# Optimization experiments

Measured on AMD Instinct MI355X. Metric: run time of the kernel, lower is better.

## Reference

```python
import jax, jax.numpy as jnp
import numpy as np

B, S, D, H = 8, 1024, 768, 12
DK = D // H  # 64


def setup_inputs() -> dict:
    key = jax.random.key(0)
    ks = jax.random.split(key, 11)
    scale = 1.0 / np.sqrt(D)
    inp = {
        "query": jax.random.normal(ks[0], (B, S, D), jnp.float32),
        "key": jax.random.normal(ks[1], (B, S, D), jnp.float32),
        "value": jax.random.normal(ks[2], (B, S, D), jnp.float32),
        "Wq": jax.random.normal(ks[3], (D, D), jnp.float32) * scale,
        "bq": jnp.zeros((D,), jnp.float32),
        "Wk": jax.random.normal(ks[4], (D, D), jnp.float32) * scale,
        "bk": jnp.zeros((D,), jnp.float32),
        "Wv": jax.random.normal(ks[5], (D, D), jnp.float32) * scale,
        "bv": jnp.zeros((D,), jnp.float32),
        "Wd": jax.random.normal(ks[6], (D, D), jnp.float32) * scale,
        "bd": jnp.zeros((D,), jnp.float32),
    }
    return inp


def reference(query, key, value, Wq, bq, Wk, bk, Wv, bv, Wd, bd):
    # QKV projections (torch Linear equivalent: x @ W + b with W stored [in,out])
    q = query @ Wq + bq  # [B,S,D]
    k = key @ Wk + bk
    v = value @ Wv + bv
    # split heads -> [B,H,S,DK]
    q = q.reshape(B, S, H, DK).transpose(0, 2, 1, 3)
    k = k.reshape(B, S, H, DK).transpose(0, 2, 1, 3)
    v = v.reshape(B, S, H, DK).transpose(0, 2, 1, 3)
    scores = jnp.einsum("bhqd,bhkd->bhqk", q, k) / jnp.sqrt(jnp.float32(DK))
    weights = jax.nn.softmax(scores, axis=-1)  # attn dropout = identity (eval)
    ctx = jnp.einsum("bhqk,bhkd->bhqd", weights, v)
    context = ctx.transpose(0, 2, 1, 3).reshape(B, S, D)
    hidden_states = context @ Wd + bd  # out dropout = identity (eval)
    return (hidden_states, context)
```

## Files before the change

kernel.cpp:

```cpp
#include <hip/hip_runtime.h>
#include <hip/hip_bf16.h>
#include <math.h>

constexpr int Bc = 8;
constexpr int Sc = 1024;
constexpr int Dc = 768;
constexpr int Hc = 12;
constexpr int DKc = 64;
constexpr int BSc = Bc * Sc;
constexpr size_t HEAD_ELEMS = (size_t)Bc * Hc * Sc * DKc;
constexpr size_t OUT_ELEMS  = (size_t)Bc * Sc * Dc;

typedef __attribute__((ext_vector_type(8))) short short8;
typedef __attribute__((ext_vector_type(4))) short short4v;
typedef __attribute__((ext_vector_type(4))) float f32x4;

__device__ __forceinline__ short f2bf(float x) {
  __hip_bfloat16 h = __float2bfloat16(x);
  short r;
  __builtin_memcpy(&r, &h, 2);
  return r;
}

__device__ __forceinline__ void gload16(const void* g, void* l) {
  __builtin_amdgcn_global_load_lds(
      (const __attribute__((address_space(1))) void*)g,
      (__attribute__((address_space(3))) void*)l, 16, 0, 0);
}

__global__ __launch_bounds__(256) void wtrans(
    const float* __restrict__ W, __hip_bfloat16* __restrict__ Wt) {
  __shared__ float t[32][33];
  const int tx = threadIdx.x & 31, ty = threadIdx.x >> 5;
  const int bx = blockIdx.x * 32;
  const int by = blockIdx.y * 32;
  #pragma unroll
  for (int i = 0; i < 32; i += 8)
    t[ty + i][tx] = W[(size_t)(by + ty + i) * Dc + bx + tx];
  __syncthreads();
  #pragma unroll
  for (int i = 0; i < 32; i += 8)
    Wt[(size_t)(bx + ty + i) * Dc + by + tx] = __float2bfloat16(t[tx][ty + i]);
}

template <int MODE>
__global__ __launch_bounds__(256) void gemm_mfma(
    const float* __restrict__ A, const __hip_bfloat16* __restrict__ Wt,
    const float* __restrict__ bias, void* __restrict__ out) {
  __shared__ __hip_bfloat16 As[128 * 64];
  __shared__ __hip_bfloat16 Bs[128 * 64];

  const int tid = threadIdx.x;
  const int lane = tid & 63;
  const int wv = tid >> 6;
  const int l15 = lane & 15;
  const int g = lane >> 4;
  const int wr = wv >> 1, wc = wv & 1;

  const int nwg = gridDim.x;
  const int orig = blockIdx.x;
  const int swz = (orig & 7) * (nwg >> 3) + (orig >> 3);
  const int rb = swz / (Dc / 128);
  const int cb = swz % (Dc / 128);
  const int row0 = rb * 128, col0 = cb * 128;

  f32x4 acc[4][4];
  #pragma unroll
  for (int ai = 0; ai < 4; ai++)
    #pragma unroll
    for (int bj = 0; bj < 4; bj++) acc[ai][bj] = f32x4{0.f, 0.f, 0.f, 0.f};

  for (int k0 = 0; k0 < Dc; k0 += 64) {
    __syncthreads();

    #pragma unroll
    for (int j = 0; j < 4; j++) {
      const int r = j * 32 + wv * 8 + (lane >> 3);
      const __hip_bfloat16* gp =
          Wt + (size_t)(col0 + r) * Dc + k0 + (lane & 7) * 8;
      gload16(gp, &Bs[(j * 32 + wv * 8) * 64]);
    }

    #pragma unroll
    for (int i = 0; i < 4; i++) {
      const int id = tid + i * 256;
      const int r = id >> 3, gi = id & 7;
      const float* ap = A + (size_t)(row0 + r) * Dc + k0 + gi * 8;
      const float4 f0 = *reinterpret_cast<const float4*>(ap);
      const float4 f1 = *reinterpret_cast<const float4*>(ap + 4);
      short8 s;
      s[0] = f2bf(f0.x); s[1] = f2bf(f0.y); s[2] = f2bf(f0.z); s[3] = f2bf(f0.w);
      s[4] = f2bf(f1.x); s[5] = f2bf(f1.y); s[6] = f2bf(f1.z); s[7] = f2bf(f1.w);
      *reinterpret_cast<short8*>(&As[r * 64 + gi * 8]) = s;
    }
    __syncthreads();

    #pragma unroll
    for (int kk = 0; kk < 2; kk++) {
      short8 a[4], b[4];
      #pragma unroll
      for (int ai = 0; ai < 4; ai++)
        a[ai] = *reinterpret_cast<const short8*>(
            &As[(wr * 64 + ai * 16 + l15) * 64 + kk * 32 + g * 8]);
      #pragma unroll
      for (int bj = 0; bj < 4; bj++)
        b[bj] = *reinterpret_cast<const short8*>(
            &Bs[(wc * 64 + bj * 16 + l15) * 64 + kk * 32 + g * 8]);
      #pragma unroll
      for (int ai = 0; ai < 4; ai++)
        #pragma unroll
        for (int bj = 0; bj < 4; bj++) {
          if constexpr (MODE == 2)
            acc[ai][bj] = __builtin_amdgcn_mfma_f32_16x16x32_bf16(
                b[bj], a[ai], acc[ai][bj], 0, 0, 0);
          else
            acc[ai][bj] = __builtin_amdgcn_mfma_f32_16x16x32_bf16(
                a[ai], b[bj], acc[ai][bj], 0, 0, 0);
        }
    }
  }

  const int mb = row0 + wr * 64, nb = col0 + wc * 64;
  #pragma unroll
  for (int ai = 0; ai < 4; ai++)
    #pragma unroll
    for (int bj = 0; bj < 4; bj++)
      #pragma unroll
      for (int reg = 0; reg < 4; reg++) {
        const float v = acc[ai][bj][reg];
        if constexpr (MODE == 2) {
          const int n = nb + bj * 16 + g * 4 + reg;
          const int m = mb + ai * 16 + l15;
          const float val = v + bias[n];
          const int b_ = m >> 10, s_ = m & 1023;
          const int h_ = n >> 6, dk = n & 63;
          ((__hip_bfloat16*)out)[(((size_t)(b_ * Hc + h_)) * DKc + dk) * Sc + s_] =
              __float2bfloat16(val);
        } else {
          const int m = mb + ai * 16 + g * 4 + reg;
          const int n = nb + bj * 16 + l15;
          const float val = v + bias[n];
          if constexpr (MODE == 0) {
            const int b_ = m >> 10, s_ = m & 1023;
            const int h_ = n >> 6, dk = n & 63;
            ((__hip_bfloat16*)out)[(((size_t)(b_ * Hc + h_)) * Sc + s_) * DKc + dk] =
                __float2bfloat16(val);
          } else {
            ((float*)out)[(size_t)m * Dc + n] = val;
          }
        }
      }
}

__global__ __launch_bounds__(256) void attn_mfma(
    const __hip_bfloat16* __restrict__ Q, const __hip_bfloat16* __restrict__ K,
    const __hip_bfloat16* __restrict__ Vt, float* __restrict__ ctx) {
  __shared__ __hip_bfloat16 Ks[64 * 64];
  __shared__ __hip_bfloat16 Vs[64 * 64];

  const int tid = threadIdx.x;
  const int lane = tid & 63;
  const int w = tid >> 6;
  const int l15 = lane & 15;
  const int g = lane >> 4;

  const int cpx = gridDim.x >> 3;
  const int bid = blockIdx.x;
  const int wid = (bid & 7) * cpx + (bid >> 3);
  const int bh = wid >> 4;
  const int qt = wid & 15;
  const int qbase = qt * 64 + w * 16;

  const __hip_bfloat16* Qb = Q + (size_t)bh * Sc * DKc;
  const __hip_bfloat16* Kb = K + (size_t)bh * Sc * DKc;
  const __hip_bfloat16* Vtb = Vt + (size_t)bh * DKc * Sc;

  short8 qf[2];
  {
    const __hip_bfloat16* qp = Qb + (size_t)(qbase + l15) * DKc + g * 8;
    qf[0] = *reinterpret_cast<const short8*>(qp);
    qf[1] = *reinterpret_cast<const short8*>(qp + 32);
  }

  f32x4 Oacc[4];
  #pragma unroll
  for (int dt = 0; dt < 4; dt++) Oacc[dt] = f32x4{0.f, 0.f, 0.f, 0.f};
  float m_run = -1e30f, l_run = 0.f;

  constexpr float SM_SCALE = 0.125f * 1.44269504088896340736f;

  for (int kt = 0; kt < Sc; kt += 64) {
    __syncthreads();
    #pragma unroll
    for (int it = 0; it < 2; it++) {
      const int tt = tid + it * 256;
      const int row = tt >> 3, s = tt & 7;
      const float4 kv = *reinterpret_cast<const float4*>(
          Kb + (size_t)(kt + row) * DKc + s * 8);
      const float4 vv = *reinterpret_cast<const float4*>(
          Vtb + (size_t)row * Sc + kt + s * 8);
      const int off = row * 128 + ((s ^ (row & 7)) << 4);
      *reinterpret_cast<float4*>((char*)Ks + off) = kv;
      *reinterpret_cast<float4*>((char*)Vs + off) = vv;
    }
    __syncthreads();

    f32x4 sacc[4];
    #pragma unroll
    for (int mt = 0; mt < 4; mt++) sacc[mt] = f32x4{0.f, 0.f, 0.f, 0.f};
    #pragma unroll
    for (int c = 0; c < 2; c++) {
      #pragma unroll
      for (int mt = 0; mt < 4; mt++) {
        const int row = mt * 16 + l15;
        const short8 kf = *reinterpret_cast<const short8*>(
            (char*)Ks + row * 128 + (((g + 4 * c) ^ (row & 7)) << 4));
        sacc[mt] =
            __builtin_amdgcn_mfma_f32_16x16x32_bf16(kf, qf[c], sacc[mt], 0, 0, 0);
      }
    }

    float tmax = -1e30f;
    #pragma unroll
    for (int s = 0; s < 4; s++)
      #pragma unroll
      for (int r = 0; r < 4; r++) tmax = fmaxf(tmax, sacc[s][r]);
    tmax = fmaxf(tmax, __shfl_xor(tmax, 16));
    tmax = fmaxf(tmax, __shfl_xor(tmax, 32));
    const float mnew = fmaxf(m_run, tmax);
    const float alpha = __builtin_amdgcn_exp2f((m_run - mnew) * SM_SCALE);
    m_run = mnew;
    float wgt[4][4];
    float wsum = 0.f;
    #pragma unroll
    for (int s = 0; s < 4; s++)
      #pragma unroll
      for (int r = 0; r < 4; r++) {
        wgt[s][r] = __builtin_amdgcn_exp2f((sacc[s][r] - mnew) * SM_SCALE);
        wsum += wgt[s][r];
      }
    l_run = l_run * alpha + wsum;

    float ar[4];
    #pragma unroll
    for (int r = 0; r < 4; r++) ar[r] = __shfl(alpha, g * 4 + r);
    #pragma unroll
    for (int dt = 0; dt < 4; dt++)
      #pragma unroll
      for (int r = 0; r < 4; r++) Oacc[dt][r] *= ar[r];

    short8 pa[2];
    #pragma unroll
    for (int c = 0; c < 2; c++)
      #pragma unroll
      for (int i = 0; i < 8; i++) pa[c][i] = f2bf(wgt[2 * c + (i >> 2)][i & 3]);

    #pragma unroll
    for (int dt = 0; dt < 4; dt++) {
      const int row = dt * 16 + l15;
      const int rb2 = row * 128;
      const int sw = row & 7;
      const int gl = (g & 1) * 8;
      const int gh = g >> 1;
      #pragma unroll
      for (int c = 0; c < 2; c++) {
        const short4v v0 = *reinterpret_cast<const short4v*>(
            (char*)Vs + rb2 + ((((4 * c + 0) + gh) ^ sw) << 4) + gl);
        const short4v v1 = *reinterpret_cast<const short4v*>(
            (char*)Vs + rb2 + ((((4 * c + 2) + gh) ^ sw) << 4) + gl);
        const short8 vf =
            __builtin_shufflevector(v0, v1, 0, 1, 2, 3, 4, 5, 6, 7);
        Oacc[dt] =
            __builtin_amdgcn_mfma_f32_16x16x32_bf16(pa[c], vf, Oacc[dt], 0, 0, 0);
      }
    }
  }

  l_run += __shfl_xor(l_run, 16);
  l_run += __shfl_xor(l_run, 32);
  float linv[4];
  #pragma unroll
  for (int r = 0; r < 4; r++) linv[r] = 1.0f / __shfl(l_run, g * 4 + r);

  const int b_ = bh / Hc, h_ = bh % Hc;
  #pragma unroll
  for (int dt = 0; dt < 4; dt++)
    #pragma unroll
    for (int r = 0; r < 4; r++) {
      const int qa = qbase + g * 4 + r;
      float* p = ctx + ((size_t)(b_ * Sc + qa)) * Dc + h_ * 64 + dt * 16 + l15;
      *p = Oacc[dt][r] * linv[r];
    }
}

extern "C" void kernel_launch(void* const* d_in, const int* in_sizes, int n_in,
                              void* d_out, int out_size, void* d_ws,
                              size_t ws_size, hipStream_t stream) {
  const float* query = (const float*)d_in[0];
  const float* key_  = (const float*)d_in[1];
  const float* value = (const float*)d_in[2];
  const float* Wq = (const float*)d_in[3];
  const float* bq = (const float*)d_in[4];
  const float* Wk = (const float*)d_in[5];
  const float* bk = (const float*)d_in[6];
  const float* Wv = (const float*)d_in[7];
  const float* bv = (const float*)d_in[8];
  const float* Wd = (const float*)d_in[9];
  const float* bd = (const float*)d_in[10];

  float* out = (float*)d_out;
  float* hidden = out;
  float* context = out + OUT_ELEMS;

  __hip_bfloat16* Qw  = (__hip_bfloat16*)d_ws;
  __hip_bfloat16* Kw  = Qw + HEAD_ELEMS;
  __hip_bfloat16* Vtw = Kw + HEAD_ELEMS;
  __hip_bfloat16* WtQ = Vtw + HEAD_ELEMS;
  __hip_bfloat16* WtK = WtQ + (size_t)Dc * Dc;
  __hip_bfloat16* WtV = WtK + (size_t)Dc * Dc;
  __hip_bfloat16* WtD = WtV + (size_t)Dc * Dc;

  const dim3 wgrid(Dc / 32, Dc / 32);
  wtrans<<<wgrid, 256, 0, stream>>>(Wq, WtQ);
  wtrans<<<wgrid, 256, 0, stream>>>(Wk, WtK);
  wtrans<<<wgrid, 256, 0, stream>>>(Wv, WtV);
  wtrans<<<wgrid, 256, 0, stream>>>(Wd, WtD);

  const int ggrid = (BSc / 128) * (Dc / 128);
  gemm_mfma<0><<<ggrid, 256, 0, stream>>>(query, WtQ, bq, Qw);
  gemm_mfma<0><<<ggrid, 256, 0, stream>>>(key_, WtK, bk, Kw);
  gemm_mfma<2><<<ggrid, 256, 0, stream>>>(value, WtV, bv, Vtw);

  attn_mfma<<<Bc * Hc * (Sc / 64), 256, 0, stream>>>(Qw, Kw, Vtw, context);

  gemm_mfma<1><<<ggrid, 256, 0, stream>>>(context, WtD, bd, hidden);
}
```

Before: 300.7 us.

## Batch weight transposes and QKV GEMMs into single launches; narrower output GEMM tiles

The four weight-transpose launches become one 3D-grid launch, and the three Q/K/V projection GEMMs become one launch indexed by blockIdx.y. The V projection epilogue now packs four consecutive sequence positions per thread into one 8-byte store instead of scattered 2-byte stores. The output projection uses a 128x64 tile to double the block count (768 instead of 384) and improve CU occupancy on the small final GEMM. The intent is to cut launch overhead and tail effects; the tradeoff is that the smaller tile reloads A more often.

```diff
diff --git a/kernel.cpp b/kernel.cpp
--- a/kernel.cpp
+++ b/kernel.cpp
@@ -28,9 +28,14 @@
       (__attribute__((address_space(3))) void*)l, 16, 0, 0);
 }
 
-__global__ __launch_bounds__(256) void wtrans(
-    const float* __restrict__ W, __hip_bfloat16* __restrict__ Wt) {
+__global__ __launch_bounds__(256) void wtrans4(
+    const float* __restrict__ W0, const float* __restrict__ W1,
+    const float* __restrict__ W2, const float* __restrict__ W3,
+    __hip_bfloat16* __restrict__ Wt0) {
   __shared__ float t[32][33];
+  const int z = blockIdx.z;
+  const float* W = (z == 0) ? W0 : (z == 1) ? W1 : (z == 2) ? W2 : W3;
+  __hip_bfloat16* Wt = Wt0 + (size_t)z * Dc * Dc;
   const int tx = threadIdx.x & 31, ty = threadIdx.x >> 5;
   const int bx = blockIdx.x * 32;
   const int by = blockIdx.y * 32;
@@ -43,10 +48,11 @@
     Wt[(size_t)(bx + ty + i) * Dc + by + tx] = __float2bfloat16(t[tx][ty + i]);
 }
 
-template <int MODE>
-__global__ __launch_bounds__(256) void gemm_mfma(
-    const float* __restrict__ A, const __hip_bfloat16* __restrict__ Wt,
-    const float* __restrict__ bias, void* __restrict__ out) {
+__global__ __launch_bounds__(256) void gemm_qkv(
+    const float* __restrict__ Aq, const float* __restrict__ Ak,
+    const float* __restrict__ Av, const __hip_bfloat16* __restrict__ Wt0,
+    const float* __restrict__ bq, const float* __restrict__ bk,
+    const float* __restrict__ bv, __hip_bfloat16* __restrict__ out0) {
   __shared__ __hip_bfloat16 As[128 * 64];
   __shared__ __hip_bfloat16 Bs[128 * 64];
 
@@ -57,9 +63,14 @@
   const int g = lane >> 4;
   const int wr = wv >> 1, wc = wv & 1;
 
-  const int nwg = gridDim.x;
+  const int proj = blockIdx.y;
+  const float* A = (proj == 0) ? Aq : (proj == 1) ? Ak : Av;
+  const float* bias = (proj == 0) ? bq : (proj == 1) ? bk : bv;
+  const __hip_bfloat16* Wt = Wt0 + (size_t)proj * Dc * Dc;
+  __hip_bfloat16* out = out0 + (size_t)proj * HEAD_ELEMS;
+
   const int orig = blockIdx.x;
-  const int swz = (orig & 7) * (nwg >> 3) + (orig >> 3);
+  const int swz = (orig & 7) * 48 + (orig >> 3);
   const int rb = swz / (Dc / 128);
   const int cb = swz % (Dc / 128);
   const int row0 = rb * 128, col0 = cb * 128;
@@ -109,47 +120,133 @@
       #pragma unroll
       for (int ai = 0; ai < 4; ai++)
         #pragma unroll
-        for (int bj = 0; bj < 4; bj++) {
-          if constexpr (MODE == 2)
-            acc[ai][bj] = __builtin_amdgcn_mfma_f32_16x16x32_bf16(
-                b[bj], a[ai], acc[ai][bj], 0, 0, 0);
-          else
-            acc[ai][bj] = __builtin_amdgcn_mfma_f32_16x16x32_bf16(
-                a[ai], b[bj], acc[ai][bj], 0, 0, 0);
+        for (int bj = 0; bj < 4; bj++)
+          acc[ai][bj] = __builtin_amdgcn_mfma_f32_16x16x32_bf16(
+              a[ai], b[bj], acc[ai][bj], 0, 0, 0);
+    }
+  }
+
+  const int mb = row0 + wr * 64, nb = col0 + wc * 64;
+  if (proj < 2) {
+    #pragma unroll
+    for (int ai = 0; ai < 4; ai++)
+      #pragma unroll
+      for (int bj = 0; bj < 4; bj++) {
+        const int n = nb + bj * 16 + l15;
+        const int h_ = n >> 6, dk = n & 63;
+        const float bn = bias[n];
+        #pragma unroll
+        for (int reg = 0; reg < 4; reg++) {
+          const int m = mb + ai * 16 + g * 4 + reg;
+          const int b_ = m >> 10, s_ = m & 1023;
+          out[(((size_t)(b_ * Hc + h_)) * Sc + s_) * DKc + dk] =
+              __float2bfloat16(acc[ai][bj][reg] + bn);
         }
-    }
+      }
+  } else {
+    #pragma unroll
+    for (int ai = 0; ai < 4; ai++)
+      #pragma unroll
+      for (int bj = 0; bj < 4; bj++) {
+        const int n = nb + bj * 16 + l15;
+        const int h_ = n >> 6, dk = n & 63;
+        const float bn = bias[n];
+        const int m0 = mb + ai * 16 + g * 4;
+        const int b_ = m0 >> 10, s0 = m0 & 1023;
+        short4v sv;
+        sv[0] = f2bf(acc[ai][bj][0] + bn);
+        sv[1] = f2bf(acc[ai][bj][1] + bn);
+        sv[2] = f2bf(acc[ai][bj][2] + bn);
+        sv[3] = f2bf(acc[ai][bj][3] + bn);
+        *reinterpret_cast<short4v*>(
+            &out[(((size_t)(b_ * Hc + h_)) * DKc + dk) * Sc + s0]) = sv;
+      }
   }
-
-  const int mb = row0 + wr * 64, nb = col0 + wc * 64;
+}
+
+__global__ __launch_bounds__(256) void gemm_out(
+    const float* __restrict__ A, const __hip_bfloat16* __restrict__ Wt,
+    const float* __restrict__ bias, float* __restrict__ out) {
+  __shared__ __hip_bfloat16 As[128 * 64];
+  __shared__ __hip_bfloat16 Bs[64 * 64];
+
+  const int tid = threadIdx.x;
+  const int lane = tid & 63;
+  const int wv = tid >> 6;
+  const int l15 = lane & 15;
+  const int g = lane >> 4;
+  const int wr = wv >> 1, wc = wv & 1;
+
+  const int orig = blockIdx.x;
+  const int swz = (orig & 7) * 96 + (orig >> 3);
+  const int rb = swz / (Dc / 64);
+  const int cb = swz % (Dc / 64);
+  const int row0 = rb * 128, col0 = cb * 64;
+
+  f32x4 acc[4][2];
   #pragma unroll
   for (int ai = 0; ai < 4; ai++)
     #pragma unroll
-    for (int bj = 0; bj < 4; bj++)
+    for (int bj = 0; bj < 2; bj++) acc[ai][bj] = f32x4{0.f, 0.f, 0.f, 0.f};
+
+  for (int k0 = 0; k0 < Dc; k0 += 64) {
+    __syncthreads();
+
+    #pragma unroll
+    for (int j = 0; j < 2; j++) {
+      const int r = j * 32 + wv * 8 + (lane >> 3);
+      const __hip_bfloat16* gp =
+          Wt + (size_t)(col0 + r) * Dc + k0 + (lane & 7) * 8;
+      gload16(gp, &Bs[(j * 32 + wv * 8) * 64]);
+    }
+
+    #pragma unroll
+    for (int i = 0; i < 4; i++) {
+      const int id = tid + i * 256;
+      const int r = id >> 3, gi = id & 7;
+      const float* ap = A + (size_t)(row0 + r) * Dc + k0 + gi * 8;
+      const float4 f0 = *reinterpret_cast<const float4*>(ap);
+      const float4 f1 = *reinterpret_cast<const float4*>(ap + 4);
+      short8 s;
+      s[0] = f2bf(f0.x); s[1] = f2bf(f0.y); s[2] = f2bf(f0.z); s[3] = f2bf(f0.w);
+      s[4] = f2bf(f1.x); s[5] = f2bf(f1.y); s[6] = f2bf(f1.z); s[7] = f2bf(f1.w);
+      *reinterpret_cast<short8*>(&As[r * 64 + gi * 8]) = s;
+    }
+    __syncthreads();
+
+    #pragma unroll
+    for (int kk = 0; kk < 2; kk++) {
+      short8 a[4], b[2];
+      #pragma unroll
+      for (int ai = 0; ai < 4; ai++)
+        a[ai] = *reinterpret_cast<const short8*>(
+            &As[(wr * 64 + ai * 16 + l15) * 64 + kk * 32 + g * 8]);
+      #pragma unroll
+      for (int bj = 0; bj < 2; bj++)
+        b[bj] = *reinterpret_cast<const short8*>(
+            &Bs[(wc * 32 + bj * 16 + l15) * 64 + kk * 32 + g * 8]);
+      #pragma unroll
+      for (int ai = 0; ai < 4; ai++)
+        #pragma unroll
+        for (int bj = 0; bj < 2; bj++)
+          acc[ai][bj] = __builtin_amdgcn_mfma_f32_16x16x32_bf16(
+              a[ai], b[bj], acc[ai][bj], 0, 0, 0);
+    }
+  }
+
+  const int mb = row0 + wr * 64, nb = col0 + wc * 32;
+  #pragma unroll
+  for (int ai = 0; ai < 4; ai++)
+    #pragma unroll
+    for (int bj = 0; bj < 2; bj++) {
+      const int n = nb + bj * 16 + l15;
+      const float bn = bias[n];
       #pragma unroll
       for (int reg = 0; reg < 4; reg++) {
-        const float v = acc[ai][bj][reg];
-        if constexpr (MODE == 2) {
-          const int n = nb + bj * 16 + g * 4 + reg;
-          const int m = mb + ai * 16 + l15;
-          const float val = v + bias[n];
-          const int b_ = m >> 10, s_ = m & 1023;
-          const int h_ = n >> 6, dk = n & 63;
-          ((__hip_bfloat16*)out)[(((size_t)(b_ * Hc + h_)) * DKc + dk) * Sc + s_] =
-              __float2bfloat16(val);
-        } else {
-          const int m = mb + ai * 16 + g * 4 + reg;
-          const int n = nb + bj * 16 + l15;
-          const float val = v + bias[n];
-          if constexpr (MODE == 0) {
-            const int b_ = m >> 10, s_ = m & 1023;
-            const int h_ = n >> 6, dk = n & 63;
-            ((__hip_bfloat16*)out)[(((size_t)(b_ * Hc + h_)) * Sc + s_) * DKc + dk] =
-                __float2bfloat16(val);
-          } else {
-            ((float*)out)[(size_t)m * Dc + n] = val;
-          }
-        }
-      }
+        const int m = mb + ai * 16 + g * 4 + reg;
+        out[(size_t)m * Dc + n] = acc[ai][bj][reg] + bn;
+      }
+    }
 }
 
 __global__ __launch_bounds__(256) void attn_mfma(
@@ -316,22 +413,15 @@
   __hip_bfloat16* Kw  = Qw + HEAD_ELEMS;
   __hip_bfloat16* Vtw = Kw + HEAD_ELEMS;
   __hip_bfloat16* WtQ = Vtw + HEAD_ELEMS;
-  __hip_bfloat16* WtK = WtQ + (size_t)Dc * Dc;
-  __hip_bfloat16* WtV = WtK + (size_t)Dc * Dc;
-  __hip_bfloat16* WtD = WtV + (size_t)Dc * Dc;
-
-  const dim3 wgrid(Dc / 32, Dc / 32);
-  wtrans<<<wgrid, 256, 0, stream>>>(Wq, WtQ);
-  wtrans<<<wgrid, 256, 0, stream>>>(Wk, WtK);
-  wtrans<<<wgrid, 256, 0, stream>>>(Wv, WtV);
-  wtrans<<<wgrid, 256, 0, stream>>>(Wd, WtD);
-
-  const int ggrid = (BSc / 128) * (Dc / 128);
-  gemm_mfma<0><<<ggrid, 256, 0, stream>>>(query, WtQ, bq, Qw);
-  gemm_mfma<0><<<ggrid, 256, 0, stream>>>(key_, WtK, bk, Kw);
-  gemm_mfma<2><<<ggrid, 256, 0, stream>>>(value, WtV, bv, Vtw);
+  __hip_bfloat16* WtD = WtQ + 3 * (size_t)Dc * Dc;
+
+  wtrans4<<<dim3(Dc / 32, Dc / 32, 4), 256, 0, stream>>>(Wq, Wk, Wv, Wd, WtQ);
+
+  gemm_qkv<<<dim3((BSc / 128) * (Dc / 128), 3), 256, 0, stream>>>(
+      query, key_, value, WtQ, bq, bk, bv, Qw);
 
   attn_mfma<<<Bc * Hc * (Sc / 64), 256, 0, stream>>>(Qw, Kw, Vtw, context);
 
-  gemm_mfma<1><<<ggrid, 256, 0, stream>>>(context, WtD, bd, hidden);
-}
+  gemm_out<<<(BSc / 128) * (Dc / 64), 256, 0, stream>>>(
+      context, WtD, bd, hidden);
+}
```

Result: faster. 289.4 us (-3.7%).
